# Performance work log

Measured on AMD Instinct MI355X. Metric: run time of the kernel, lower is better.

Reference implementation:

```python
import jax, jax.numpy as jnp
import numpy as np
from jax import lax

T, B = 256, 64
VOCAB, EMB, HID, NLAB = 100000, 300, 256, 20
PAD_WORD = 0


def setup_inputs() -> dict:
    key = jax.random.key(0)
    ks = jax.random.split(key, 16)
    sentences = jax.random.randint(ks[0], (T, B), 0, VOCAB)
    sentences = sentences.at[0].set(jnp.maximum(sentences[0], 1))  # mask[0] must be all on (torchcrf)
    labels = jax.random.randint(ks[1], (T, B), 0, NLAB)
    s = 0.05
    emb = jax.random.normal(ks[2], (VOCAB, EMB), jnp.float32) * s
    Wih_f = jax.random.normal(ks[3], (4 * HID, EMB), jnp.float32) * s
    Whh_f = jax.random.normal(ks[4], (4 * HID, HID), jnp.float32) * s
    b_f = jax.random.normal(ks[5], (4 * HID,), jnp.float32) * s
    Wih_b = jax.random.normal(ks[6], (4 * HID, EMB), jnp.float32) * s
    Whh_b = jax.random.normal(ks[7], (4 * HID, HID), jnp.float32) * s
    b_b = jax.random.normal(ks[8], (4 * HID,), jnp.float32) * s
    W_top = jax.random.normal(ks[9], (NLAB, 2 * HID), jnp.float32) * s
    b_top = jax.random.normal(ks[10], (NLAB,), jnp.float32) * s
    start_t = jax.random.normal(ks[11], (NLAB,), jnp.float32) * 0.1
    end_t = jax.random.normal(ks[12], (NLAB,), jnp.float32) * 0.1
    trans = jax.random.normal(ks[13], (NLAB, NLAB), jnp.float32) * 0.1
    return dict(emb=emb, Wih_f=Wih_f, Whh_f=Whh_f, b_f=b_f, Wih_b=Wih_b,
                Whh_b=Whh_b, b_b=b_b, W_top=W_top, b_top=b_top,
                start_t=start_t, end_t=end_t, trans=trans,
                sentences=sentences, labels=labels)


def _lstm_dir(x, W_ih, W_hh, b, reverse):
    # x: (T, B, E) -> hs: (T, B, H); torch gate order i,f,g,o
    H = W_hh.shape[1]
    x_proj = jnp.einsum('tbe,ge->tbg', x, W_ih) + b  # precompute input projection

    def step(carry, xp):
        h, c = carry
        gates = xp + h @ W_hh.T
        i, f, g, o = jnp.split(gates, 4, axis=-1)
        c = jax.nn.sigmoid(f) * c + jax.nn.sigmoid(i) * jnp.tanh(g)
        h = jax.nn.sigmoid(o) * jnp.tanh(c)
        return (h, c), h

    init = (jnp.zeros((x.shape[1], H), x.dtype), jnp.zeros((x.shape[1], H), x.dtype))
    _, hs = lax.scan(step, init, x_proj, reverse=reverse)
    return hs


def _crf_nll(emissions, tags, mask, start_t, end_t, trans):
    # emissions: (T,B,L), tags: (T,B), mask: (T,B) bool. torchcrf math, reduction='sum'.
    Tn, Bn, L = emissions.shape
    maskf = mask.astype(emissions.dtype)
    barange = jnp.arange(Bn)
    # numerator
    score = start_t[tags[0]] + emissions[0, barange, tags[0]]
    trans_sc = trans[tags[:-1], tags[1:]]  # (T-1, B)
    emit_sc = jnp.take_along_axis(emissions[1:], tags[1:, :, None], axis=2)[..., 0]
    score = score + ((trans_sc + emit_sc) * maskf[1:]).sum(0)
    seq_ends = mask.astype(jnp.int32).sum(0) - 1  # (B,)
    last_tags = jnp.take_along_axis(tags, seq_ends[None, :], axis=0)[0]
    score = score + end_t[last_tags]
    # partition (log-sum-exp forward recurrence)
    alpha0 = start_t[None, :] + emissions[0]  # (B, L)

    def step(alpha, inp):
        emis_t, m_t = inp
        nxt = jax.nn.logsumexp(alpha[:, :, None] + trans[None] + emis_t[:, None, :], axis=1)
        return jnp.where(m_t[:, None], nxt, alpha), None

    alpha, _ = lax.scan(step, alpha0, (emissions[1:], mask[1:]))
    denom = jax.nn.logsumexp(alpha + end_t[None, :], axis=1)
    llh = (score - denom).sum()
    return -llh


def reference(emb, Wih_f, Whh_f, b_f, Wih_b, Whh_b, b_b, W_top, b_top,
              start_t, end_t, trans, sentences, labels):
    x = emb[sentences]  # (T, B, E)
    h_f = _lstm_dir(x, Wih_f, Whh_f, b_f, reverse=False)
    h_b = _lstm_dir(x, Wih_b, Whh_b, b_b, reverse=True)
    rnn_out = jnp.concatenate([h_f, h_b], axis=-1)  # (T, B, 2H)
    emissions = jnp.einsum('tbh,lh->tbl', rnn_out, W_top) + b_top
    mask = sentences != PAD_WORD
    return _crf_nll(emissions, labels, mask, start_t, end_t, trans)
```

## Files before the change

kernel.cpp:

```cpp
#include <hip/hip_runtime.h>
#include <hip/hip_bf16.h>

#define T_    256
#define B_    64
#define EMB_  300
#define HID_  256
#define G_    1024
#define L_    20
#define M_    (T_*B_)

#define NCL   32
#define CLB   8
#define BPC   4
#define UPB   32

typedef float f32x4 __attribute__((ext_vector_type(4)));

__global__ __launch_bounds__(256) void k_xproj(
    const float* __restrict__ emb,
    const float* __restrict__ Wih_f, const float* __restrict__ b_f,
    const float* __restrict__ Wih_b, const float* __restrict__ b_b,
    const int*   __restrict__ sent,
    float* __restrict__ xp)
{
    __shared__ float As[16][68];
    __shared__ float Bs[16][68];
    __shared__ int   words[64];

    const int tid = threadIdx.x;
    const int n0  = blockIdx.x * 64;
    const int m0  = blockIdx.y * 64;
    const int dir = n0 >> 10;
    const int g0  = n0 & 1023;
    const float* __restrict__ Wih  = dir ? Wih_b : Wih_f;
    const float* __restrict__ bias = dir ? b_b   : b_f;

    if (tid < 64) words[tid] = sent[m0 + tid];
    __syncthreads();

    const int r = tid >> 2;
    const int q = tid & 3;
    const float* aptr = emb + (size_t)words[r] * EMB_ + q * 4;
    const float* bptr = Wih + (size_t)(g0 + r) * EMB_ + q * 4;

    const int tx = tid & 15;
    const int ty = tid >> 4;
    float acc[4][4] = {};

    for (int k0 = 0; k0 < 304; k0 += 16) {
        const int k = k0 + q * 4;
        float4 av = make_float4(0.f, 0.f, 0.f, 0.f);
        float4 bv = make_float4(0.f, 0.f, 0.f, 0.f);
        if (k < 300) {
            av = *(const float4*)(aptr + k0);
            bv = *(const float4*)(bptr + k0);
        }
        As[q*4+0][r] = av.x; As[q*4+1][r] = av.y; As[q*4+2][r] = av.z; As[q*4+3][r] = av.w;
        Bs[q*4+0][r] = bv.x; Bs[q*4+1][r] = bv.y; Bs[q*4+2][r] = bv.z; Bs[q*4+3][r] = bv.w;
        __syncthreads();
        #pragma unroll
        for (int kk = 0; kk < 16; ++kk) {
            const float4 a = *(const float4*)&As[kk][ty * 4];
            const float4 b = *(const float4*)&Bs[kk][tx * 4];
            acc[0][0] += a.x*b.x; acc[0][1] += a.x*b.y; acc[0][2] += a.x*b.z; acc[0][3] += a.x*b.w;
            acc[1][0] += a.y*b.x; acc[1][1] += a.y*b.y; acc[1][2] += a.y*b.z; acc[1][3] += a.y*b.w;
            acc[2][0] += a.z*b.x; acc[2][1] += a.z*b.y; acc[2][2] += a.z*b.z; acc[2][3] += a.z*b.w;
            acc[3][0] += a.w*b.x; acc[3][1] += a.w*b.y; acc[3][2] += a.w*b.z; acc[3][3] += a.w*b.w;
        }
        __syncthreads();
    }

    float* out = xp + (size_t)dir * M_ * G_;
    const int g = g0 + tx * 4;
    const float4 bs4 = *(const float4*)(bias + g);
    #pragma unroll
    for (int im = 0; im < 4; ++im) {
        const int m = m0 + ty * 4 + im;
        float4 rv;
        rv.x = acc[im][0] + bs4.x;
        rv.y = acc[im][1] + bs4.y;
        rv.z = acc[im][2] + bs4.z;
        rv.w = acc[im][3] + bs4.w;
        *(float4*)(out + (size_t)m * G_ + g) = rv;
    }
}

__global__ __launch_bounds__(256, 1) void k_lstm_scan(
    const float* __restrict__ Whh_f, const float* __restrict__ Whh_b,
    const float* __restrict__ xp, float* __restrict__ hbuf,
    int* __restrict__ flags)
{
    const int rank = blockIdx.x & 7;
    const int cl   = blockIdx.x >> 3;
    const int dir  = cl >> 4;
    const int bg   = cl & 15;
    const int b0   = bg * BPC;
    const int u0   = rank * UPB;
    const int tid  = threadIdx.x;
    const int lane = tid & 63;
    const int g    = tid >> 6;
    const int r32  = lane & 31;
    const int kh   = lane >> 5;

    const float* __restrict__ Whh = dir ? Whh_b : Whh_f;
    const float* __restrict__ xpd = xp + (size_t)dir * M_ * G_;
    float* __restrict__ hdir = hbuf + (size_t)dir * M_ * HID_;
    int* __restrict__ myflags = flags + cl * 16;

    __shared__ float hs[BPC][264];
    __shared__ float Cg[4][UPB][BPC+1];
    __shared__ float cs[BPC][UPB + 1];

    for (int i = tid; i < BPC * 264; i += 256) ((float*)hs)[i] = 0.f;
    if (tid < BPC * (UPB + 1)) ((float*)cs)[tid] = 0.f;

    f32x4 wv[32];
    {
        const f32x4* wrow = (const f32x4*)(Whh + (size_t)(g * HID_ + u0 + r32) * HID_ + kh * 128);
        #pragma unroll
        for (int i = 0; i < 32; ++i) wv[i] = wrow[i];
    }
    __syncthreads();

    const int eu = tid & 31;
    const int eb = tid >> 5;

    for (int t = 0; t < T_; ++t) {
        const int t_eff = dir ? (T_ - 1 - t) : t;

        #pragma unroll
        for (int i = 0; i < 32; ++i) asm volatile("" : "+v"(wv[i]));

        float x0 = 0.f, x1 = 0.f, x2 = 0.f, x3 = 0.f;
        if (tid < 128) {
            const float* xrow = xpd + ((size_t)t_eff * B_ + (b0 + eb)) * G_ + (u0 + eu);
            x0 = xrow[0]; x1 = xrow[HID_]; x2 = xrow[2 * HID_]; x3 = xrow[3 * HID_];
        }

        #pragma unroll
        for (int b = 0; b < BPC; ++b) {
            const f32x4* hv = (const f32x4*)&hs[b][kh * 132];
            float acc = 0.f;
            #pragma unroll
            for (int i = 0; i < 32; ++i) {
                const f32x4 w4 = wv[i];
                const f32x4 h4 = hv[i];
                acc += w4.x * h4.x + w4.y * h4.y + w4.z * h4.z + w4.w * h4.w;
            }
            acc += __shfl_xor(acc, 32);
            if (kh == 0) Cg[g][r32][b] = acc;
        }
        __syncthreads();

        if (tid < 128) {
            const float gi = Cg[0][eu][eb] + x0;
            const float gf = Cg[1][eu][eb] + x1;
            const float gg = Cg[2][eu][eb] + x2;
            const float go = Cg[3][eu][eb] + x3;
            const float i_ = 1.f / (1.f + __expf(-gi));
            const float f_ = 1.f / (1.f + __expf(-gf));
            const float g_ = tanhf(gg);
            const float o_ = 1.f / (1.f + __expf(-go));
            const float cn = f_ * cs[eb][eu] + i_ * g_;
            const float hn = o_ * tanhf(cn);
            cs[eb][eu] = cn;
            __hip_atomic_store(
                &hdir[((size_t)t_eff * B_ + (b0 + eb)) * HID_ + (u0 + eu)],
                hn, __ATOMIC_RELAXED, __HIP_MEMORY_SCOPE_AGENT);
        }
        __syncthreads();

        if (t == T_ - 1) break;

        if (tid == 0)
            __hip_atomic_store(&myflags[rank], t + 1,
                               __ATOMIC_RELAXED, __HIP_MEMORY_SCOPE_AGENT);
        if (tid < 64) {
            while (true) {
                int v = (tid < CLB)
                    ? __hip_atomic_load(&myflags[tid], __ATOMIC_RELAXED,
                                        __HIP_MEMORY_SCOPE_AGENT)
                    : 0x7FFFFFFF;
                if (__ballot(v <= t) == 0ULL) break;
                __builtin_amdgcn_s_sleep(1);
            }
        }
        __syncthreads();

        {
            const float* hsrc = hdir + ((size_t)t_eff * B_ + b0) * HID_;
            #pragma unroll
            for (int i = 0; i < 4; ++i) {
                const int idx = i * 256 + tid;
                const int b = idx >> 8, k = idx & 255;
                const float v = __hip_atomic_load(hsrc + (size_t)b * HID_ + k,
                                                  __ATOMIC_RELAXED,
                                                  __HIP_MEMORY_SCOPE_AGENT);
                hs[b][(k >> 7) * 132 + (k & 127)] = v;
            }
        }
        __syncthreads();
    }
}

__global__ __launch_bounds__(256) void k_emis(
    const float* __restrict__ Wt, const float* __restrict__ bt,
    const float* __restrict__ hbuf, float* __restrict__ em)
{
    const int gid = blockIdx.x * 256 + threadIdx.x;
    if (gid >= M_ * L_) return;
    const int m = gid / L_;
    const int l = gid - m * L_;
    const float4* hf  = (const float4*)(hbuf + (size_t)m * HID_);
    const float4* hbk = (const float4*)(hbuf + (size_t)M_ * HID_ + (size_t)m * HID_);
    const float4* w0  = (const float4*)(Wt + (size_t)l * 2 * HID_);
    const float4* w1  = w0 + HID_ / 4;
    float acc = bt[l];
    #pragma unroll 4
    for (int k = 0; k < HID_ / 4; ++k) {
        float4 h = hf[k],  w = w0[k];
        acc += h.x*w.x + h.y*w.y + h.z*w.z + h.w*w.w;
        h = hbk[k]; w = w1[k];
        acc += h.x*w.x + h.y*w.y + h.z*w.z + h.w*w.w;
    }
    em[gid] = acc;
}

__global__ __launch_bounds__(64) void k_crf(
    const float* __restrict__ start_t, const float* __restrict__ end_t,
    const float* __restrict__ trans,
    const int* __restrict__ sent, const int* __restrict__ labels,
    const float* __restrict__ em, float* __restrict__ res)
{
    const int b = blockIdx.x;
    const int tid = threadIdx.x;
    __shared__ float tr[L_ * L_];
    __shared__ float alpha[2][L_];
    __shared__ float red[64];
    __shared__ int   redi[64];
    __shared__ float sdenom;

    for (int i = tid; i < L_ * L_; i += 64) tr[i] = trans[i];
    if (tid < L_) alpha[0][tid] = start_t[tid] + em[b * L_ + tid];
    __syncthreads();

    float pre_em = (tid < L_) ? em[(B_ + b) * L_ + tid] : 0.f;
    int   pre_m  = sent[B_ + b];

    int p = 0;
    for (int t = 1; t < T_; ++t) {
        const float emt = pre_em;
        const int   mt  = pre_m;
        if (t + 1 < T_) {
            if (tid < L_) pre_em = em[((t + 1) * B_ + b) * L_ + tid];
            pre_m = sent[(t + 1) * B_ + b];
        }
        float val = 0.f;
        if (tid < L_) {
            if (mt != 0) {
                float mx = -1e30f;
                #pragma unroll
                for (int i = 0; i < L_; ++i) mx = fmaxf(mx, alpha[p][i] + tr[i * L_ + tid]);
                float s = 0.f;
                #pragma unroll
                for (int i = 0; i < L_; ++i) s += __expf(alpha[p][i] + tr[i * L_ + tid] - mx);
                val = mx + __logf(s) + emt;
            } else {
                val = alpha[p][tid];
            }
        }
        if (tid < L_) alpha[1 - p][tid] = val;
        __syncthreads();
        p ^= 1;
    }

    if (tid == 0) {
        float mx = -1e30f;
        for (int j = 0; j < L_; ++j) mx = fmaxf(mx, alpha[p][j] + end_t[j]);
        float s = 0.f;
        for (int j = 0; j < L_; ++j) s += __expf(alpha[p][j] + end_t[j] - mx);
        sdenom = mx + __logf(s);
    }

    float loc = 0.f;
    int   cnt = 0;
    for (int t = tid; t < T_; t += 64) {
        const int masked = (sent[t * B_ + b] != 0);
        cnt += masked;
        if (t >= 1 && masked) {
            const int tp = labels[(t - 1) * B_ + b];
            const int tc = labels[t * B_ + b];
            loc += tr[tp * L_ + tc] + em[(t * B_ + b) * L_ + tc];
        }
    }
    red[tid] = loc; redi[tid] = cnt;
    __syncthreads();
    if (tid == 0) {
        float s = 0.f; int c = 0;
        for (int i = 0; i < 64; ++i) { s += red[i]; c += redi[i]; }
        const int tag0 = labels[b];
        const int seq_end = c - 1;
        const int last = labels[seq_end * B_ + b];
        const float score = start_t[tag0] + em[b * L_ + tag0] + s + end_t[last];
        res[b] = score - sdenom;
    }
}

__global__ __launch_bounds__(64) void k_final(const float* __restrict__ res,
                                              float* __restrict__ out)
{
    __shared__ float red[64];
    red[threadIdx.x] = res[threadIdx.x];
    __syncthreads();
    if (threadIdx.x == 0) {
        float s = 0.f;
        for (int i = 0; i < 64; ++i) s += red[i];
        out[0] = -s;
    }
}

extern "C" void kernel_launch(void* const* d_in, const int* in_sizes, int n_in,
                              void* d_out, int out_size, void* d_ws, size_t ws_size,
                              hipStream_t stream)
{
    const float* emb     = (const float*)d_in[0];
    const float* Wih_f   = (const float*)d_in[1];
    const float* Whh_f   = (const float*)d_in[2];
    const float* b_f     = (const float*)d_in[3];
    const float* Wih_b   = (const float*)d_in[4];
    const float* Whh_b   = (const float*)d_in[5];
    const float* b_b     = (const float*)d_in[6];
    const float* W_top   = (const float*)d_in[7];
    const float* b_top   = (const float*)d_in[8];
    const float* start_t = (const float*)d_in[9];
    const float* end_t   = (const float*)d_in[10];
    const float* trans   = (const float*)d_in[11];
    const int*   sent    = (const int*)d_in[12];
    const int*   labels  = (const int*)d_in[13];
    float* out = (float*)d_out;

    float* wsf  = (float*)d_ws;
    float* xp   = wsf;
    float* hbuf = xp   + (size_t)2 * M_ * G_;
    float* em   = hbuf + (size_t)2 * M_ * HID_;
    float* res  = em   + (size_t)M_ * L_;
    int*   flags = (int*)(res + 64);

    hipMemsetAsync(flags, 0, NCL * 16 * sizeof(int), stream);

    k_xproj<<<dim3(2048 / 64, M_ / 64), 256, 0, stream>>>(
        emb, Wih_f, b_f, Wih_b, b_b, sent, xp);

    {
        void* args[] = { (void*)&Whh_f, (void*)&Whh_b, (void*)&xp, (void*)&hbuf, (void*)&flags };
        hipLaunchCooperativeKernel((const void*)k_lstm_scan, dim3(256), dim3(256),
                                   args, 0, stream);
    }

    k_emis<<<(M_ * L_ + 255) / 256, 256, 0, stream>>>(W_top, b_top, hbuf, em);

    k_crf<<<B_, 64, 0, stream>>>(start_t, end_t, trans, sent, labels, em, res);

    k_final<<<1, 64, 0, stream>>>(res, out);
}
```

Before: 2.044 ms.

## Replace flag barrier with tagged 64-bit value exchange in LSTM scan

The scan kernel no longer publishes hidden states and then raises per-rank flags that every block spins on. Each hidden value is now stored together with its step number in a single 64-bit atomic word. Consumers poll those words directly until the tag matches, which removes the separate flag round trip and one block barrier per step. The trade-off is 8-byte traffic per hidden element, and correctness now relies on stale tags from a previous call or an uninitialised workspace never matching the step being waited on.

```diff
diff --git a/kernel.cpp b/kernel.cpp
--- a/kernel.cpp
+++ b/kernel.cpp
@@ -15,6 +15,7 @@
 #define UPB   32
 
 typedef float f32x4 __attribute__((ext_vector_type(4)));
+typedef unsigned long long u64;
 
 __global__ __launch_bounds__(256) void k_xproj(
     const float* __restrict__ emb,
@@ -88,7 +89,7 @@
 __global__ __launch_bounds__(256, 1) void k_lstm_scan(
     const float* __restrict__ Whh_f, const float* __restrict__ Whh_b,
     const float* __restrict__ xp, float* __restrict__ hbuf,
-    int* __restrict__ flags)
+    u64* __restrict__ xch)
 {
     const int rank = blockIdx.x & 7;
     const int cl   = blockIdx.x >> 3;
@@ -105,7 +106,7 @@
     const float* __restrict__ Whh = dir ? Whh_b : Whh_f;
     const float* __restrict__ xpd = xp + (size_t)dir * M_ * G_;
     float* __restrict__ hdir = hbuf + (size_t)dir * M_ * HID_;
-    int* __restrict__ myflags = flags + cl * 16;
+    u64* __restrict__ xc = xch + ((size_t)dir * B_ + b0) * HID_;
 
     __shared__ float hs[BPC][264];
     __shared__ float Cg[4][UPB][BPC+1];
@@ -125,6 +126,13 @@
     const int eu = tid & 31;
     const int eb = tid >> 5;
 
+    int pb[4], pk[4];
+    #pragma unroll
+    for (int i = 0; i < 4; ++i) {
+        const int idx = i * 256 + tid;
+        pb[i] = idx >> 8; pk[i] = idx & 255;
+    }
+
     for (int t = 0; t < T_; ++t) {
         const int t_eff = dir ? (T_ - 1 - t) : t;
 
@@ -136,6 +144,28 @@
             const float* xrow = xpd + ((size_t)t_eff * B_ + (b0 + eb)) * G_ + (u0 + eu);
             x0 = xrow[0]; x1 = xrow[HID_]; x2 = xrow[2 * HID_]; x3 = xrow[3 * HID_];
         }
+
+        if (t > 0) {
+            const unsigned want = (unsigned)t;
+            u64 v[4];
+            #pragma unroll
+            for (int i = 0; i < 4; ++i)
+                v[i] = __hip_atomic_load(&xc[(size_t)pb[i] * HID_ + pk[i]],
+                                         __ATOMIC_RELAXED, __HIP_MEMORY_SCOPE_AGENT);
+            while ((unsigned)(v[0] >> 32) != want || (unsigned)(v[1] >> 32) != want ||
+                   (unsigned)(v[2] >> 32) != want || (unsigned)(v[3] >> 32) != want) {
+                #pragma unroll
+                for (int i = 0; i < 4; ++i)
+                    if ((unsigned)(v[i] >> 32) != want)
+                        v[i] = __hip_atomic_load(&xc[(size_t)pb[i] * HID_ + pk[i]],
+                                                 __ATOMIC_RELAXED, __HIP_MEMORY_SCOPE_AGENT);
+            }
+            #pragma unroll
+            for (int i = 0; i < 4; ++i)
+                hs[pb[i]][(pk[i] >> 7) * 132 + (pk[i] & 127)] =
+                    __uint_as_float((unsigned)v[i]);
+        }
+        __syncthreads();
 
         #pragma unroll
         for (int b = 0; b < BPC; ++b) {
@@ -164,42 +194,13 @@
             const float cn = f_ * cs[eb][eu] + i_ * g_;
             const float hn = o_ * tanhf(cn);
             cs[eb][eu] = cn;
-            __hip_atomic_store(
-                &hdir[((size_t)t_eff * B_ + (b0 + eb)) * HID_ + (u0 + eu)],
-                hn, __ATOMIC_RELAXED, __HIP_MEMORY_SCOPE_AGENT);
-        }
-        __syncthreads();
-
-        if (t == T_ - 1) break;
-
-        if (tid == 0)
-            __hip_atomic_store(&myflags[rank], t + 1,
-                               __ATOMIC_RELAXED, __HIP_MEMORY_SCOPE_AGENT);
-        if (tid < 64) {
-            while (true) {
-                int v = (tid < CLB)
-                    ? __hip_atomic_load(&myflags[tid], __ATOMIC_RELAXED,
-                                        __HIP_MEMORY_SCOPE_AGENT)
-                    : 0x7FFFFFFF;
-                if (__ballot(v <= t) == 0ULL) break;
-                __builtin_amdgcn_s_sleep(1);
+            if (t + 1 < T_) {
+                const u64 pkv = ((u64)(unsigned)(t + 1) << 32) | __float_as_uint(hn);
+                __hip_atomic_store(&xc[(size_t)eb * HID_ + (u0 + eu)], pkv,
+                                   __ATOMIC_RELAXED, __HIP_MEMORY_SCOPE_AGENT);
             }
-        }
-        __syncthreads();
-
-        {
-            const float* hsrc = hdir + ((size_t)t_eff * B_ + b0) * HID_;
-            #pragma unroll
-            for (int i = 0; i < 4; ++i) {
-                const int idx = i * 256 + tid;
-                const int b = idx >> 8, k = idx & 255;
-                const float v = __hip_atomic_load(hsrc + (size_t)b * HID_ + k,
-                                                  __ATOMIC_RELAXED,
-                                                  __HIP_MEMORY_SCOPE_AGENT);
-                hs[b][(k >> 7) * 132 + (k & 127)] = v;
-            }
-        }
-        __syncthreads();
+            hdir[((size_t)t_eff * B_ + (b0 + eb)) * HID_ + (u0 + eu)] = hn;
+        }
     }
 }
 
@@ -344,15 +345,13 @@
     float* hbuf = xp   + (size_t)2 * M_ * G_;
     float* em   = hbuf + (size_t)2 * M_ * HID_;
     float* res  = em   + (size_t)M_ * L_;
-    int*   flags = (int*)(res + 64);
-
-    hipMemsetAsync(flags, 0, NCL * 16 * sizeof(int), stream);
+    u64*   xch  = (u64*)(res + 64);
 
     k_xproj<<<dim3(2048 / 64, M_ / 64), 256, 0, stream>>>(
         emb, Wih_f, b_f, Wih_b, b_b, sent, xp);
 
     {
-        void* args[] = { (void*)&Whh_f, (void*)&Whh_b, (void*)&xp, (void*)&hbuf, (void*)&flags };
+        void* args[] = { (void*)&Whh_f, (void*)&Whh_b, (void*)&xp, (void*)&hbuf, (void*)&xch };
         hipLaunchCooperativeKernel((const void*)k_lstm_scan, dim3(256), dim3(256),
                                    args, 0, stream);
     }
```

Result: faster. 1.846 ms (-9.7%).
